# Kernel optimization log

Hardware: AMD Instinct MI355X
Metric: run time of the kernel (lower is better)

## Reference

```python
import jax, jax.numpy as jnp
import numpy as np


def _conv(x, w, b, dilation=1):
    # NCHW conv with 'same' padding scaled by dilation (matches default_conv)
    k = w.shape[2]
    pad = dilation * (k // 2)
    y = jax.lax.conv_general_dilated(
        x, w, window_strides=(1, 1), padding=[(pad, pad), (pad, pad)],
        rhs_dilation=(dilation, dilation),
        dimension_numbers=('NCHW', 'OIHW', 'NCHW'))
    return y + b[None, :, None, None]


def setup_inputs() -> dict:
    key = jax.random.key(0)
    ks = jax.random.split(key, 24)
    B, S, C, H, W = 4, 8, 128, 128, 128
    r = lambda k, sh, s=0.1: jax.random.normal(k, sh, jnp.float32) * s
    return {
        'x': jax.random.normal(ks[0], (B, S, H, W), jnp.float32),
        'd1w': r(ks[1], (C, S, 3, 3)), 'd1b': r(ks[2], (C,)),
        'd4w': r(ks[3], (C, S, 3, 3)), 'd4b': r(ks[4], (C,)),
        'pa': jnp.full((1,), 0.25, jnp.float32),
        'f1w1': r(ks[5], (C, C, 1, 1)), 'f1b1': r(ks[6], (C,)),
        'f1w2': r(ks[7], (C, C, 1, 1)), 'f1b2': r(ks[8], (C,)),
        'f2w1': r(ks[9], (C, C, 1, 1)), 'f2b1': r(ks[10], (C,)),
        'f2w2': r(ks[11], (C, C, 1, 1)), 'f2b2': r(ks[12], (C,)),
        'pw1': r(ks[13], (2 * C, C, 1, 1)), 'pb1': r(ks[14], (2 * C,)),
        'pw2': r(ks[15], (C, 2 * C, 1, 1)), 'pb2': r(ks[16], (C,)),
        'pw3': r(ks[17], (C, C, 1, 1)), 'pb3': r(ks[18], (C,)),
    }


def _forward(x, d1w, d1b, d4w, d4b, pa,
             f1w1, f1b1, f1w2, f1b2, f2w1, f2b1, f2w2, f2b2,
             pw1, pb1, pw2, pb2, pw3, pb3):
    # ---- DPB: dilated conv branches (dil 1 and 7), shared PReLU, sum ----
    x1 = _conv(x, d1w, d1b, 1)
    x1 = jnp.where(x1 >= 0, x1, pa * x1)
    x4 = _conv(x, d4w, d4b, 7)
    x4 = jnp.where(x4 >= 0, x4, pa * x4)
    y1 = x1 + x4  # [B,C,H,W]

    # ---- MHSA: gated SRU-style recurrence over height (reverse=True) ----
    Z = jnp.tanh(_conv(jnp.tanh(_conv(y1, f1w1, f1b1)), f1w2, f1b2))
    Fg = jax.nn.sigmoid(_conv(jnp.tanh(_conv(y1, f2w1, f2b1)), f2w2, f2b2))
    C = Z.shape[1]
    Ch = C // 2
    # multi-head: second half of channels scans in the opposite direction
    Z = jnp.concatenate([Z[:, :Ch], jnp.flip(Z[:, Ch:], 2)], 1)
    Fg = jnp.concatenate([Fg[:, :Ch], jnp.flip(Fg[:, Ch:], 2)], 1)
    Zs = jnp.moveaxis(Z, 2, 0)   # [H,B,C,W]
    Fs = jnp.moveaxis(Fg, 2, 0)

    def step(h, zf):
        z, f = zf
        h = f * h + (1.0 - f) * z
        return h, h

    _, hs = jax.lax.scan(step, jnp.zeros_like(Zs[0]), (Zs, Fs), reverse=True)
    y2 = jnp.moveaxis(hs, 0, 2)  # [B,C,H,W], original H order
    y2 = jnp.concatenate([y2[:, :Ch], jnp.flip(y2[:, Ch:], 2)], 1)

    # ---- PSA: progressive spectral channel attention ----
    p = _conv(y1, pw3, pb3) * y1 + y1
    p = jax.nn.gelu(_conv(p, pw1, pb1), approximate=False)
    y3 = _conv(p, pw2, pb2)

    return y1 * jax.nn.sigmoid(y2) + y3


def reference(x, d1w, d1b, d4w, d4b, pa,
              f1w1, f1b1, f1w2, f1b2, f2w1, f2b1, f2w2, f2b2,
              pw1, pb1, pw2, pb2, pw3, pb3):
    return _forward(x, d1w, d1b, d4w, d4b, pa,
                    f1w1, f1b1, f1w2, f1b2, f2w1, f2b1, f2w2, f2b2,
                    pw1, pb1, pw2, pb2, pw3, pb3)
```

## Files before the change

### kernel.cpp

```cpp
#include <hip/hip_runtime.h>


typedef __bf16 bf16x8 __attribute__((ext_vector_type(8)));
typedef __bf16 bf16x4 __attribute__((ext_vector_type(4)));
typedef __bf16 bf16x2 __attribute__((ext_vector_type(2)));
typedef float  f32x4  __attribute__((ext_vector_type(4)));

constexpr int kHW = 16384;

__device__ __align__(16) __bf16 g_y1[8388608];
__device__ __align__(16) __bf16 g_ZF[16777216];
__device__ __align__(16) __bf16 g_S [8388608];
__device__ __align__(16) __bf16 g_w [172032];

__device__ __forceinline__ float hw_exp2(float x)
{
    float r;
    asm("v_exp_f32 %0, %1" : "=v"(r) : "v"(x));
    return r;
}
__device__ __forceinline__ float hw_rcp(float x)
{
    float r;
    asm("v_rcp_f32 %0, %1" : "=v"(r) : "v"(x));
    return r;
}
__device__ __forceinline__ float fast_tanh(float x)
{
    return 1.f - 2.f * hw_rcp(hw_exp2(2.88539008f * x) + 1.f);
}
__device__ __forceinline__ float fast_sig(float x)
{
    return hw_rcp(1.f + hw_exp2(-1.44269504f * x));
}
__device__ __forceinline__ float fast_gelu(float x)
{
    return 0.5f * x * (1.f + fast_tanh(0.79788456f * (x + 0.044715f * x * x * x)));
}

__global__ __launch_bounds__(256) void k_prepw(
    const float* __restrict__ f1w1, const float* __restrict__ f1w2,
    const float* __restrict__ f2w1, const float* __restrict__ f2w2,
    const float* __restrict__ pw1, const float* __restrict__ pw2,
    const float* __restrict__ d1w, const float* __restrict__ d4w,
    const float* __restrict__ pw3)
{
    int idx = blockIdx.x * 256 + threadIdx.x;
    float v;
    if (idx < 16384)        v = f1w1[idx];
    else if (idx < 32768)   v = f1w2[idx - 16384];
    else if (idx < 49152)   v = f2w1[idx - 32768];
    else if (idx < 65536)   v = f2w2[idx - 49152];
    else if (idx < 98304)   v = pw1[idx - 65536];
    else if (idx < 131072)  v = pw2[idx - 98304];
    else if (idx < 155648) {
        int r = idx - 131072;
        const float* src = d1w;
        if (r >= 12288) { r -= 12288; src = d4w; }
        int c = r / 96, k = r - c * 96;
        int tap = k >> 3, s = k & 7;
        v = (tap < 9) ? src[c * 72 + s * 9 + tap] : 0.f;
    } else                  v = pw3[idx - 155648];
    g_w[idx] = (__bf16)v;
}

__global__ __launch_bounds__(512) void k_fused(
    const float* __restrict__ x, const float* __restrict__ d1b,
    const float* __restrict__ d4b, const float* __restrict__ pa,
    const float* __restrict__ f1b1, const float* __restrict__ f1b2,
    const float* __restrict__ f2b1, const float* __restrict__ f2b2)
{
    __shared__ __align__(16) char U1[17408];
    __shared__ __align__(16) char U2[17408];
    auto Bt    = (__bf16 (*)[136])U1;
    auto Tz    = (__bf16 (*)[136])U1;
    auto patch = (__bf16 (*)[80][8])U2;
    auto Tf    = (__bf16 (*)[136])U2;

    const int tid = threadIdx.x;
    const int n0 = blockIdx.x * 64;
    const int b = n0 >> 14, hw0 = n0 & 16383;
    const int h = hw0 >> 7, w0 = hw0 & 127;

    const int roff[5] = {-7, -1, 0, 1, 7};
    if (tid < 400) {
        int rs = tid / 80, c = tid - rs * 80;
        int row = h + roff[rs], wc = w0 + c - 7;
        bf16x8 v;
#pragma unroll
        for (int s = 0; s < 8; ++s) v[s] = (__bf16)0.f;
        if ((unsigned)row < 128u && (unsigned)wc < 128u && c < 78) {
#pragma unroll
            for (int s = 0; s < 8; ++s)
                v[s] = (__bf16)x[(size_t)(b * 8 + s) * kHW + row * 128 + wc];
        }
        *(bf16x8*)&patch[rs][c][0] = v;
    }

    const int lane = tid & 63, wid = tid >> 6;
    const int fr = lane & 15, kg = (lane >> 4) << 3, mrow = (lane >> 4) << 2;
    const int mbase = wid * 16;

    f32x4 acc1[4], acc4[4];
#pragma unroll
    for (int nt = 0; nt < 4; ++nt)
#pragma unroll
        for (int r = 0; r < 4; ++r) { acc1[nt][r] = 0.f; acc4[nt][r] = 0.f; }

    __syncthreads();

#pragma unroll
    for (int cv = 0; cv < 2; ++cv) {
        const __bf16* Ag = g_w + (cv ? 143360 : 131072);
#pragma unroll
        for (int k0 = 0; k0 < 96; k0 += 32) {
            bf16x8 af = *(const bf16x8*)&Ag[(size_t)(mbase + fr) * 96 + k0 + kg];
            int tap = (k0 + kg) >> 3;
            bf16x8 bfr[4];
#pragma unroll
            for (int nt = 0; nt < 4; ++nt) {
                bf16x8 bv;
#pragma unroll
                for (int i = 0; i < 8; ++i) bv[i] = (__bf16)0.f;
                if (tap < 9) {
                    int dh = tap / 3 - 1, dw = tap % 3 - 1;
                    int rowsel = cv ? (dh + 1) * 2 : dh + 2;
                    int col = nt * 16 + fr + dw * (cv ? 7 : 1) + 7;
                    bv = *(const bf16x8*)&patch[rowsel][col][0];
                }
                bfr[nt] = bv;
            }
            if (cv == 0) {
#pragma unroll
                for (int nt = 0; nt < 4; ++nt)
                    acc1[nt] = __builtin_amdgcn_mfma_f32_16x16x32_bf16(af, bfr[nt], acc1[nt], 0, 0, 0);
            } else {
#pragma unroll
                for (int nt = 0; nt < 4; ++nt)
                    acc4[nt] = __builtin_amdgcn_mfma_f32_16x16x32_bf16(af, bfr[nt], acc4[nt], 0, 0, 0);
            }
        }
    }

    __syncthreads();

    const float pav = pa[0];
    {
        int m = mbase + mrow;
        f32x4 b1v = *(const f32x4*)&d1b[m];
        f32x4 b4v = *(const f32x4*)&d4b[m];
#pragma unroll
        for (int nt = 0; nt < 4; ++nt) {
            int nl = nt * 16 + fr;
            bf16x4 o;
#pragma unroll
            for (int r = 0; r < 4; ++r) {
                float v1 = acc1[nt][r] + b1v[r];
                float v4 = acc4[nt][r] + b4v[r];
                v1 = (v1 >= 0.f) ? v1 : pav * v1;
                v4 = (v4 >= 0.f) ? v4 : pav * v4;
                o[r] = (__bf16)(v1 + v4);
            }
            *(bf16x4*)&Bt[nl][m] = o;
            *(bf16x4*)&g_y1[(size_t)(n0 + nl) * 128 + m] = o;
        }
    }
    __syncthreads();

    {
        f32x4 az[4], afc[4];
#pragma unroll
        for (int nt = 0; nt < 4; ++nt)
#pragma unroll
            for (int r = 0; r < 4; ++r) { az[nt][r] = 0.f; afc[nt][r] = 0.f; }
#pragma unroll
        for (int k0 = 0; k0 < 128; k0 += 32) {
            size_t rowoff = (size_t)(mbase + fr) * 128 + k0 + kg;
            bf16x8 wz = *(const bf16x8*)&g_w[rowoff];
            bf16x8 wf = *(const bf16x8*)&g_w[32768 + rowoff];
            bf16x8 bfr[4];
#pragma unroll
            for (int nt = 0; nt < 4; ++nt)
                bfr[nt] = *(const bf16x8*)&Bt[nt * 16 + fr][k0 + kg];
#pragma unroll
            for (int nt = 0; nt < 4; ++nt) {
                az[nt]  = __builtin_amdgcn_mfma_f32_16x16x32_bf16(wz, bfr[nt], az[nt], 0, 0, 0);
                afc[nt] = __builtin_amdgcn_mfma_f32_16x16x32_bf16(wf, bfr[nt], afc[nt], 0, 0, 0);
            }
        }
        __syncthreads();
        int m = mbase + mrow;
        f32x4 bz = *(const f32x4*)&f1b1[m];
        f32x4 bfv = *(const f32x4*)&f2b1[m];
#pragma unroll
        for (int nt = 0; nt < 4; ++nt) {
            int nl = nt * 16 + fr;
            bf16x4 oz, of;
#pragma unroll
            for (int r = 0; r < 4; ++r) {
                oz[r] = (__bf16)fast_tanh(az[nt][r] + bz[r]);
                of[r] = (__bf16)fast_tanh(afc[nt][r] + bfv[r]);
            }
            *(bf16x4*)&Tz[nl][m] = oz;
            *(bf16x4*)&Tf[nl][m] = of;
        }
    }
    __syncthreads();

    {
        f32x4 az[4], afc[4];
#pragma unroll
        for (int nt = 0; nt < 4; ++nt)
#pragma unroll
            for (int r = 0; r < 4; ++r) { az[nt][r] = 0.f; afc[nt][r] = 0.f; }
#pragma unroll
        for (int k0 = 0; k0 < 128; k0 += 32) {
            size_t rowoff = (size_t)(mbase + fr) * 128 + k0 + kg;
            bf16x8 wz = *(const bf16x8*)&g_w[16384 + rowoff];
            bf16x8 wf = *(const bf16x8*)&g_w[49152 + rowoff];
            bf16x8 bz[4], bf[4];
#pragma unroll
            for (int nt = 0; nt < 4; ++nt) {
                bz[nt] = *(const bf16x8*)&Tz[nt * 16 + fr][k0 + kg];
                bf[nt] = *(const bf16x8*)&Tf[nt * 16 + fr][k0 + kg];
            }
#pragma unroll
            for (int nt = 0; nt < 4; ++nt) {
                az[nt]  = __builtin_amdgcn_mfma_f32_16x16x32_bf16(wz, bz[nt], az[nt], 0, 0, 0);
                afc[nt] = __builtin_amdgcn_mfma_f32_16x16x32_bf16(wf, bf[nt], afc[nt], 0, 0, 0);
            }
        }
        int m = mbase + mrow;
        f32x4 bz = *(const f32x4*)&f1b2[m];
        f32x4 bfv = *(const f32x4*)&f2b2[m];
#pragma unroll
        for (int nt = 0; nt < 4; ++nt) {
            int nl = nt * 16 + fr;
            bf16x8 ozf;
#pragma unroll
            for (int r = 0; r < 4; ++r) {
                ozf[2 * r]     = (__bf16)fast_tanh(az[nt][r] + bz[r]);
                ozf[2 * r + 1] = (__bf16)fast_sig(afc[nt][r] + bfv[r]);
            }
            *(bf16x8*)&g_ZF[(size_t)(n0 + nl) * 256 + 2 * m] = ozf;
        }
    }
}

__global__ __launch_bounds__(256) void k_scan()
{
    int b = blockIdx.x >> 6;
    int w = ((blockIdx.x & 63) << 1) + (threadIdx.x >> 7);
    int c = threadIdx.x & 127;
    size_t pix0 = (size_t)(b * kHW + w);
    float st = 0.f;
    if (c < 64) {
#pragma unroll 8
        for (int h = 127; h >= 0; --h) {
            size_t pix = pix0 + (size_t)h * 128;
            bf16x2 v = *(const bf16x2*)&g_ZF[pix * 256 + 2 * c];
            float z = (float)v[0], f = (float)v[1];
            st = f * st + (1.f - f) * z;
            g_S[pix * 128 + c] = (__bf16)fast_sig(st);
        }
    } else {
#pragma unroll 8
        for (int h = 0; h < 128; ++h) {
            size_t pix = pix0 + (size_t)h * 128;
            bf16x2 v = *(const bf16x2*)&g_ZF[pix * 256 + 2 * c];
            float z = (float)v[0], f = (float)v[1];
            st = f * st + (1.f - f) * z;
            g_S[pix * 128 + c] = (__bf16)fast_sig(st);
        }
    }
}

__global__ __launch_bounds__(512) void k_mega(
    const float* __restrict__ pb3, const float* __restrict__ pb1,
    const float* __restrict__ pb2, float* __restrict__ out)
{
    __shared__ __align__(16) char U[34816];
    auto Bt = (__bf16 (*)[136])U;
    auto Pt = (__bf16 (*)[136])(U + 17408);
    auto Qt = (__bf16 (*)[264])U;

    const int tid = threadIdx.x;
    const int n0 = blockIdx.x * 64;
    const int b = n0 >> 14, hw0 = n0 & 16383;
    const int lane = tid & 63, wid = tid >> 6;
    const int fr = lane & 15, kg = (lane >> 4) << 3, mrow = (lane >> 4) << 2;
    const int mbase = wid * 16;

    {
        int n = tid >> 3, ks = (tid & 7) * 16;
        const __bf16* src = g_y1 + (size_t)(n0 + n) * 128 + ks;
        *(bf16x8*)&Bt[n][ks]     = *(const bf16x8*)src;
        *(bf16x8*)&Bt[n][ks + 8] = *(const bf16x8*)(src + 8);
    }
    __syncthreads();

    {
        f32x4 acc[4];
#pragma unroll
        for (int nt = 0; nt < 4; ++nt)
#pragma unroll
            for (int r = 0; r < 4; ++r) acc[nt][r] = 0.f;
#pragma unroll
        for (int k0 = 0; k0 < 128; k0 += 32) {
            bf16x8 af = *(const bf16x8*)&g_w[155648 + (size_t)(mbase + fr) * 128 + k0 + kg];
            bf16x8 bfr[4];
#pragma unroll
            for (int nt = 0; nt < 4; ++nt)
                bfr[nt] = *(const bf16x8*)&Bt[nt * 16 + fr][k0 + kg];
#pragma unroll
            for (int nt = 0; nt < 4; ++nt)
                acc[nt] = __builtin_amdgcn_mfma_f32_16x16x32_bf16(af, bfr[nt], acc[nt], 0, 0, 0);
        }
        int m = mbase + mrow;
        f32x4 b3 = *(const f32x4*)&pb3[m];
#pragma unroll
        for (int nt = 0; nt < 4; ++nt) {
            int nl = nt * 16 + fr;
            bf16x4 yv = *(const bf16x4*)&Bt[nl][m];
            bf16x4 o;
#pragma unroll
            for (int r = 0; r < 4; ++r) {
                float y = (float)yv[r];
                o[r] = (__bf16)((acc[nt][r] + b3[r]) * y + y);
            }
            *(bf16x4*)&Pt[nl][m] = o;
        }
    }
    __syncthreads();

    {
        f32x4 acc[2][4];
#pragma unroll
        for (int mh = 0; mh < 2; ++mh)
#pragma unroll
            for (int nt = 0; nt < 4; ++nt)
#pragma unroll
                for (int r = 0; r < 4; ++r) acc[mh][nt][r] = 0.f;
#pragma unroll
        for (int mh = 0; mh < 2; ++mh) {
#pragma unroll
            for (int k0 = 0; k0 < 128; k0 += 32) {
                bf16x8 af = *(const bf16x8*)&g_w[65536 + (size_t)(mh * 128 + mbase + fr) * 128 + k0 + kg];
                bf16x8 bfr[4];
#pragma unroll
                for (int nt = 0; nt < 4; ++nt)
                    bfr[nt] = *(const bf16x8*)&Pt[nt * 16 + fr][k0 + kg];
#pragma unroll
                for (int nt = 0; nt < 4; ++nt)
                    acc[mh][nt] = __builtin_amdgcn_mfma_f32_16x16x32_bf16(af, bfr[nt], acc[mh][nt], 0, 0, 0);
            }
        }
        __syncthreads();
#pragma unroll
        for (int mh = 0; mh < 2; ++mh) {
            int m = mh * 128 + mbase + mrow;
            f32x4 b1 = *(const f32x4*)&pb1[m];
#pragma unroll
            for (int nt = 0; nt < 4; ++nt) {
                int nl = nt * 16 + fr;
                bf16x4 o;
#pragma unroll
                for (int r = 0; r < 4; ++r)
                    o[r] = (__bf16)fast_gelu(acc[mh][nt][r] + b1[r]);
                *(bf16x4*)&Qt[nl][m] = o;
            }
        }
    }
    __syncthreads();

    {
        f32x4 acc[4];
#pragma unroll
        for (int nt = 0; nt < 4; ++nt)
#pragma unroll
            for (int r = 0; r < 4; ++r) acc[nt][r] = 0.f;
#pragma unroll
        for (int k0 = 0; k0 < 256; k0 += 32) {
            bf16x8 af = *(const bf16x8*)&g_w[98304 + (size_t)(mbase + fr) * 256 + k0 + kg];
            bf16x8 bfr[4];
#pragma unroll
            for (int nt = 0; nt < 4; ++nt)
                bfr[nt] = *(const bf16x8*)&Qt[nt * 16 + fr][k0 + kg];
#pragma unroll
            for (int nt = 0; nt < 4; ++nt)
                acc[nt] = __builtin_amdgcn_mfma_f32_16x16x32_bf16(af, bfr[nt], acc[nt], 0, 0, 0);
        }
        int m = mbase + mrow;
        f32x4 b2 = *(const f32x4*)&pb2[m];
#pragma unroll
        for (int nt = 0; nt < 4; ++nt) {
            int hw = hw0 + nt * 16 + fr;
            size_t pbase = (size_t)(n0 + nt * 16 + fr) * 128;
            bf16x4 yv = *(const bf16x4*)&g_y1[pbase + m];
            bf16x4 sv = *(const bf16x4*)&g_S[pbase + m];
#pragma unroll
            for (int r = 0; r < 4; ++r) {
                out[(size_t)(b * 128 + m + r) * kHW + hw] =
                    acc[nt][r] + b2[r] + (float)yv[r] * (float)sv[r];
            }
        }
    }
}

extern "C" void kernel_launch(void* const* d_in, const int* in_sizes, int n_in,
                              void* d_out, int out_size, void* d_ws, size_t ws_size,
                              hipStream_t stream)
{
    const float* x    = (const float*)d_in[0];
    const float* d1w  = (const float*)d_in[1];
    const float* d1b  = (const float*)d_in[2];
    const float* d4w  = (const float*)d_in[3];
    const float* d4b  = (const float*)d_in[4];
    const float* pa   = (const float*)d_in[5];
    const float* f1w1 = (const float*)d_in[6];
    const float* f1b1 = (const float*)d_in[7];
    const float* f1w2 = (const float*)d_in[8];
    const float* f1b2 = (const float*)d_in[9];
    const float* f2w1 = (const float*)d_in[10];
    const float* f2b1 = (const float*)d_in[11];
    const float* f2w2 = (const float*)d_in[12];
    const float* f2b2 = (const float*)d_in[13];
    const float* pw1  = (const float*)d_in[14];
    const float* pb1  = (const float*)d_in[15];
    const float* pw2  = (const float*)d_in[16];
    const float* pb2  = (const float*)d_in[17];
    const float* pw3  = (const float*)d_in[18];
    const float* pb3  = (const float*)d_in[19];
    float* out = (float*)d_out;

    k_prepw<<<672, 256, 0, stream>>>(f1w1, f1w2, f2w1, f2w2, pw1, pw2, d1w, d4w, pw3);
    k_fused<<<1024, 512, 0, stream>>>(x, d1b, d4b, pa, f1b1, f1b2, f2b1, f2b2);
    k_scan<<<256, 256, 0, stream>>>();
    k_mega<<<1024, 512, 0, stream>>>(pb3, pb1, pb2, out);

    (void)in_sizes; (void)n_in; (void)d_ws; (void)ws_size; (void)out_size;
}
```

Measured before the change: 91.39 us.

## Parallelize height scan into chunked affine scan and drop y1 LDS staging

The sequential 128-step scan per column is split into four 32-row chunks per thread group. Each chunk computes an affine composition (A, B), and these are combined in shared memory before each chunk replays its rows from the correct starting state. This raises the grid from 256 to 1024 blocks and shortens the serial dependency chain, at the cost of holding 64 floats per thread in registers. Separately, k_mega now reads y1 fragments directly from global memory instead of staging them in LDS, which removes a sync and shrinks shared memory but may add redundant global loads.

```diff
diff --git a/kernel.cpp b/kernel.cpp
--- a/kernel.cpp
+++ b/kernel.cpp
@@ -247,31 +247,55 @@
     }
 }
 
-__global__ __launch_bounds__(256) void k_scan()
-{
-    int b = blockIdx.x >> 6;
-    int w = ((blockIdx.x & 63) << 1) + (threadIdx.x >> 7);
-    int c = threadIdx.x & 127;
-    size_t pix0 = (size_t)(b * kHW + w);
-    float st = 0.f;
-    if (c < 64) {
-#pragma unroll 8
-        for (int h = 127; h >= 0; --h) {
-            size_t pix = pix0 + (size_t)h * 128;
-            bf16x2 v = *(const bf16x2*)&g_ZF[pix * 256 + 2 * c];
-            float z = (float)v[0], f = (float)v[1];
-            st = f * st + (1.f - f) * z;
-            g_S[pix * 128 + c] = (__bf16)fast_sig(st);
-        }
-    } else {
-#pragma unroll 8
-        for (int h = 0; h < 128; ++h) {
-            size_t pix = pix0 + (size_t)h * 128;
-            bf16x2 v = *(const bf16x2*)&g_ZF[pix * 256 + 2 * c];
-            float z = (float)v[0], f = (float)v[1];
-            st = f * st + (1.f - f) * z;
-            g_S[pix * 128 + c] = (__bf16)fast_sig(st);
-        }
+__global__ __launch_bounds__(256) void k_scan_par()
+{
+    __shared__ float sA[4][64], sB[4][64], sS[4][64];
+
+    const int bid = blockIdx.x;
+    const int bw = bid >> 1;
+    const int cg = bid & 1;
+    const int b = bw >> 7, w = bw & 127;
+    const int tid = threadIdx.x;
+    const int q = tid >> 6, cl = tid & 63;
+    const int c = cg * 64 + cl;
+    const bool rev = (cg == 0);
+    const size_t colbase = (size_t)(b * kHW) + w;
+
+    float zb[32], fb[32];
+    float A = 1.f, Bv = 0.f;
+#pragma unroll
+    for (int i = 0; i < 32; ++i) {
+        int t = q * 32 + i;
+        int hh = rev ? (127 - t) : t;
+        size_t pix = colbase + (size_t)hh * 128;
+        bf16x2 v = *(const bf16x2*)&g_ZF[pix * 256 + 2 * c];
+        float z = (float)v[0], f = (float)v[1];
+        zb[i] = z; fb[i] = f;
+        A = f * A;
+        Bv = f * Bv + (1.f - f) * z;
+    }
+    sA[q][cl] = A;
+    sB[q][cl] = Bv;
+    __syncthreads();
+
+    if (q == 0) {
+        float S = 0.f;
+#pragma unroll
+        for (int j = 0; j < 4; ++j) {
+            sS[j][cl] = S;
+            S = sA[j][cl] * S + sB[j][cl];
+        }
+    }
+    __syncthreads();
+
+    float st = sS[q][cl];
+#pragma unroll
+    for (int i = 0; i < 32; ++i) {
+        int t = q * 32 + i;
+        int hh = rev ? (127 - t) : t;
+        size_t pix = colbase + (size_t)hh * 128;
+        st = fb[i] * st + (1.f - fb[i]) * zb[i];
+        g_S[pix * 128 + c] = (__bf16)fast_sig(st);
     }
 }
 
@@ -279,9 +303,8 @@
     const float* __restrict__ pb3, const float* __restrict__ pb1,
     const float* __restrict__ pb2, float* __restrict__ out)
 {
-    __shared__ __align__(16) char U[34816];
-    auto Bt = (__bf16 (*)[136])U;
-    auto Pt = (__bf16 (*)[136])(U + 17408);
+    __shared__ __align__(16) char U[33792];
+    auto Pt = (__bf16 (*)[136])U;
     auto Qt = (__bf16 (*)[264])U;
 
     const int tid = threadIdx.x;
@@ -292,14 +315,6 @@
     const int mbase = wid * 16;
 
     {
-        int n = tid >> 3, ks = (tid & 7) * 16;
-        const __bf16* src = g_y1 + (size_t)(n0 + n) * 128 + ks;
-        *(bf16x8*)&Bt[n][ks]     = *(const bf16x8*)src;
-        *(bf16x8*)&Bt[n][ks + 8] = *(const bf16x8*)(src + 8);
-    }
-    __syncthreads();
-
-    {
         f32x4 acc[4];
 #pragma unroll
         for (int nt = 0; nt < 4; ++nt)
@@ -311,7 +326,7 @@
             bf16x8 bfr[4];
 #pragma unroll
             for (int nt = 0; nt < 4; ++nt)
-                bfr[nt] = *(const bf16x8*)&Bt[nt * 16 + fr][k0 + kg];
+                bfr[nt] = *(const bf16x8*)&g_y1[(size_t)(n0 + nt * 16 + fr) * 128 + k0 + kg];
 #pragma unroll
             for (int nt = 0; nt < 4; ++nt)
                 acc[nt] = __builtin_amdgcn_mfma_f32_16x16x32_bf16(af, bfr[nt], acc[nt], 0, 0, 0);
@@ -321,7 +336,7 @@
 #pragma unroll
         for (int nt = 0; nt < 4; ++nt) {
             int nl = nt * 16 + fr;
-            bf16x4 yv = *(const bf16x4*)&Bt[nl][m];
+            bf16x4 yv = *(const bf16x4*)&g_y1[(size_t)(n0 + nl) * 128 + m];
             bf16x4 o;
 #pragma unroll
             for (int r = 0; r < 4; ++r) {
@@ -435,7 +450,7 @@
 
     k_prepw<<<672, 256, 0, stream>>>(f1w1, f1w2, f2w1, f2w2, pw1, pw2, d1w, d4w, pw3);
     k_fused<<<1024, 512, 0, stream>>>(x, d1b, d4b, pa, f1b1, f1b2, f2b1, f2b2);
-    k_scan<<<256, 256, 0, stream>>>();
+    k_scan_par<<<1024, 256, 0, stream>>>();
     k_mega<<<1024, 512, 0, stream>>>(pb3, pb1, pb2, out);
 
     (void)in_sizes; (void)n_in; (void)d_ws; (void)ws_size; (void)out_size;
```

Result: slower. 105.2 us (+15.1%).
